# Kernel optimization log

Hardware: AMD Instinct MI355X
Metric: run time of the kernel (lower is better)

## Reference

```python
import jax, jax.numpy as jnp
import numpy as np


def setup_inputs() -> dict:
    key = jax.random.key(0)
    k1, k2 = jax.random.split(key)
    B, N, M = 4, 16384, 4096
    src_points = jax.random.normal(k1, (B, N, 3), dtype=jnp.float32)
    target_verts = jax.random.normal(k2, (B, M, 3), dtype=jnp.float32)
    return {"src_points": src_points, "target_verts": target_verts}


def reference(src_points, target_verts):
    # target_faces=None path of ChamferLoss: degenerate one-vertex triangles,
    # so closest-point-on-mesh == nearest target vertex.
    # d2[b,n,m] = ||p_bn - v_bm||^2 via the expansion p2 + v2 - 2 p.v
    p2 = jnp.sum(src_points * src_points, axis=-1)          # (B, N)
    v2 = jnp.sum(target_verts * target_verts, axis=-1)      # (B, M)
    pv = jnp.einsum('bnd,bmd->bnm', src_points, target_verts)  # (B, N, M)
    d2 = p2[:, :, None] + v2[:, None, :] - 2.0 * pv
    d2 = jnp.maximum(d2, 0.0)
    min_d2 = jnp.min(d2, axis=-1)                            # (B, N)
    num_src_per_batch = src_points.shape[1]
    loss = jnp.sum(min_d2, axis=-1) / num_src_per_batch      # (B,)
    return loss
```

## Files before the change

### kernel.cpp

```cpp
#include <hip/hip_runtime.h>
#include <float.h>


typedef __bf16 bf16x8 __attribute__((ext_vector_type(8)));
typedef float  f32x16 __attribute__((ext_vector_type(16)));

constexpr int B = 4, N = 16384, M = 4096;
constexpr int BN = B * N;
constexpr int TPB = 512;
constexpr int PPB = 256;
constexpr int NPB = BN / PPB;
constexpr int CHUNK = 2048;
constexpr int NCH = M / CHUNK;
constexpr int CT = CHUNK / 32;
constexpr int HT = CT / 2;

__global__ __launch_bounds__(TPB) void chamfer_fused(
    const float* __restrict__ src, const float* __restrict__ tv,
    float* __restrict__ out)
{
    __shared__ uint4 lds4[4096];
    char* ldsc = (char*)lds4;

    const int pblk = blockIdx.x;
    const int b    = pblk >> 6;
    const int t    = threadIdx.x;
    const int w    = t >> 6, L = t & 63;
    const int s    = w & 3, h = w >> 2;
    const int half = L >> 5, c = L & 31;
    const int laneoff = half * 512 + c * 16;

    const int P0 = pblk * PPB + s * 64;
    const int p0 = P0 + c, p1 = P0 + 32 + c;
    float x0 = src[3 * p0], y0 = src[3 * p0 + 1], z0 = src[3 * p0 + 2];
    float x1 = src[3 * p1], y1 = src[3 * p1 + 1], z1 = src[3 * p1 + 2];
    float pp0 = fmaf(x0, x0, fmaf(y0, y0, z0 * z0));
    float pp1 = fmaf(x1, x1, fmaf(y1, y1, z1 * z1));

    __bf16 one = (__bf16)1.0f, zero = (__bf16)0.0f;
    bf16x8 bP0, bP1;
    {
        __bf16 xh = (__bf16)x0, yh = (__bf16)y0, zh = (__bf16)z0;
        __bf16 xl = (__bf16)(x0 - (float)xh), yl = (__bf16)(y0 - (float)yh),
               zl = (__bf16)(z0 - (float)zh);
        if (half == 0) { bP0[0]=xh; bP0[1]=yh; bP0[2]=zh; bP0[3]=xl; bP0[4]=yl; bP0[5]=zl; bP0[6]=xh; bP0[7]=yh; }
        else { bP0[0]=zh; bP0[1]=one; bP0[2]=one; bP0[3]=zero; bP0[4]=zero; bP0[5]=zero; bP0[6]=zero; bP0[7]=zero; }
    }
    {
        __bf16 xh = (__bf16)x1, yh = (__bf16)y1, zh = (__bf16)z1;
        __bf16 xl = (__bf16)(x1 - (float)xh), yl = (__bf16)(y1 - (float)yh),
               zl = (__bf16)(z1 - (float)zh);
        if (half == 0) { bP1[0]=xh; bP1[1]=yh; bP1[2]=zh; bP1[3]=xl; bP1[4]=yl; bP1[5]=zl; bP1[6]=xh; bP1[7]=yh; }
        else { bP1[0]=zh; bP1[1]=one; bP1[2]=one; bP1[3]=zero; bP1[4]=zero; bP1[5]=zero; bP1[6]=zero; bP1[7]=zero; }
    }

    f32x16 zeroC;
#pragma unroll
    for (int r = 0; r < 16; ++r) zeroC[r] = 0.0f;
    float mn0[8], mn1[8];
#pragma unroll
    for (int u = 0; u < 8; ++u) { mn0[u] = FLT_MAX; mn1[u] = FLT_MAX; }

    for (int ch = 0; ch < NCH; ++ch) {
        if (ch) __syncthreads();

#pragma unroll
        for (int k = 0; k < 4; ++k) {
            int ml = t + k * 512;
            int i  = b * M + ch * CHUNK + ml;
            float x = tv[3 * i + 0], y = tv[3 * i + 1], z = tv[3 * i + 2];
            __bf16 xh = (__bf16)x, yh = (__bf16)y, zh = (__bf16)z;
            float xhf = (float)xh, yhf = (float)yh, zhf = (float)zh;
            __bf16 xl = (__bf16)(x - xhf), yl = (__bf16)(y - yhf),
                   zl = (__bf16)(z - zhf);
            float v2 = fmaf(x, x, fmaf(y, y, z * z));
            __bf16 v2h = (__bf16)v2;
            __bf16 v2l = (__bf16)(v2 - (float)v2h);

            bf16x8 h0, h1;
            h0[0] = (__bf16)(-2.0f * xhf); h0[1] = (__bf16)(-2.0f * yhf);
            h0[2] = (__bf16)(-2.0f * zhf);
            h0[3] = h0[0]; h0[4] = h0[1]; h0[5] = h0[2];
            h0[6] = (__bf16)(-2.0f * (float)xl); h0[7] = (__bf16)(-2.0f * (float)yl);
            h1[0] = (__bf16)(-2.0f * (float)zl); h1[1] = v2h; h1[2] = v2l;
            h1[3] = zero; h1[4] = zero; h1[5] = zero; h1[6] = zero; h1[7] = zero;

            size_t base = (size_t)(ml >> 5) * 1024 + (size_t)(ml & 31) * 16;
            *(bf16x8*)(ldsc + base)       = h0;
            *(bf16x8*)(ldsc + base + 512) = h1;
        }
        __syncthreads();

        const char* abase = ldsc + (size_t)h * (HT * 1024) + laneoff;
#pragma unroll 8
        for (int tt = 0; tt < HT; ++tt) {
            bf16x8 av = *(const bf16x8*)(abase + tt * 1024);
            f32x16 C0 = __builtin_amdgcn_mfma_f32_32x32x16_bf16(av, bP0, zeroC, 0, 0, 0);
            f32x16 C1 = __builtin_amdgcn_mfma_f32_32x32x16_bf16(av, bP1, zeroC, 0, 0, 0);
#pragma unroll
            for (int u = 0; u < 8; ++u) {
                mn0[u] = fminf(fminf(mn0[u], C0[2 * u]), C0[2 * u + 1]);
                mn1[u] = fminf(fminf(mn1[u], C1[2 * u]), C1[2 * u + 1]);
            }
        }
    }

    float a01 = fminf(fminf(mn0[0], mn0[1]), fminf(mn0[2], mn0[3]));
    float a23 = fminf(fminf(mn0[4], mn0[5]), fminf(mn0[6], mn0[7]));
    float m0 = fminf(a01, a23);
    m0 = fminf(m0, __shfl_xor(m0, 32, 64));
    float b01 = fminf(fminf(mn1[0], mn1[1]), fminf(mn1[2], mn1[3]));
    float b23 = fminf(fminf(mn1[4], mn1[5]), fminf(mn1[6], mn1[7]));
    float m1 = fminf(b01, b23);
    m1 = fminf(m1, __shfl_xor(m1, 32, 64));
    float m  = half ? m1 : m0;
    float pp = half ? pp1 : pp0;

    __syncthreads();
    float* lf = (float*)ldsc;
    float* acc = lf + 512;
    lf[t] = m;
    __syncthreads();

    float sum = 0.0f;
    if (w < 4) {
        float mm = fminf(m, lf[t + 256]);
        sum = fmaxf(mm + pp, 0.0f);
    }
    for (int off = 32; off > 0; off >>= 1)
        sum += __shfl_down(sum, off, 64);
    if (L == 0) acc[w] = sum;
    __syncthreads();
    if (t == 0) {
        float ssum = acc[0] + acc[1] + acc[2] + acc[3];
        atomicAdd(&out[b], ssum * (1.0f / N));
    }
}

extern "C" void kernel_launch(void* const* d_in, const int* in_sizes, int n_in,
                              void* d_out, int out_size, void* d_ws, size_t ws_size,
                              hipStream_t stream) {
    const float* src = (const float*)d_in[0];
    const float* tv  = (const float*)d_in[1];
    float* out = (float*)d_out;

    hipMemsetAsync(out, 0, out_size, stream);
    chamfer_fused<<<NPB, TPB, 0, stream>>>(src, tv, out);
}
```

Measured before the change: 66.83 us.

## Replace memset+atomics with cooperative grid sync reduction and prefetch next chunk

Drops the hipMemsetAsync and per-block atomicAdd. Each block now writes its partial sum to workspace, the grid synchronizes cooperatively, and the first B blocks reduce the partials into the output. It also prefetches the next chunk's target vertices into registers while the current chunk is computed. The aim is to remove a separate memset launch and to hide global load latency. The cost is a cooperative launch with a grid barrier, which requires all 256 blocks to be resident at once, plus extra registers for the prefetch.

```diff
diff --git a/kernel.cpp b/kernel.cpp
--- a/kernel.cpp
+++ b/kernel.cpp
@@ -1,5 +1,8 @@
 #include <hip/hip_runtime.h>
+#include <hip/hip_cooperative_groups.h>
 #include <float.h>
+
+namespace cg = cooperative_groups;
 
 
 typedef __bf16 bf16x8 __attribute__((ext_vector_type(8)));
@@ -15,9 +18,9 @@
 constexpr int CT = CHUNK / 32;
 constexpr int HT = CT / 2;
 
-__global__ __launch_bounds__(TPB) void chamfer_fused(
+__global__ __launch_bounds__(TPB) void chamfer_coop(
     const float* __restrict__ src, const float* __restrict__ tv,
-    float* __restrict__ out)
+    float* __restrict__ bs, float* __restrict__ out)
 {
     __shared__ uint4 lds4[4096];
     char* ldsc = (char*)lds4;
@@ -61,14 +64,21 @@
 #pragma unroll
     for (int u = 0; u < 8; ++u) { mn0[u] = FLT_MAX; mn1[u] = FLT_MAX; }
 
+    float cx[4], cy[4], cz[4], nx[4], ny[4], nz[4];
+#pragma unroll
+    for (int k = 0; k < 4; ++k) {
+        int i = b * M + t + k * 512;
+        cx[k] = tv[3 * i + 0]; cy[k] = tv[3 * i + 1]; cz[k] = tv[3 * i + 2];
+    }
+
+#pragma unroll
     for (int ch = 0; ch < NCH; ++ch) {
         if (ch) __syncthreads();
 
 #pragma unroll
         for (int k = 0; k < 4; ++k) {
             int ml = t + k * 512;
-            int i  = b * M + ch * CHUNK + ml;
-            float x = tv[3 * i + 0], y = tv[3 * i + 1], z = tv[3 * i + 2];
+            float x = cx[k], y = cy[k], z = cz[k];
             __bf16 xh = (__bf16)x, yh = (__bf16)y, zh = (__bf16)z;
             float xhf = (float)xh, yhf = (float)yh, zhf = (float)zh;
             __bf16 xl = (__bf16)(x - xhf), yl = (__bf16)(y - yhf),
@@ -89,6 +99,14 @@
             *(bf16x8*)(ldsc + base)       = h0;
             *(bf16x8*)(ldsc + base + 512) = h1;
         }
+
+        if (ch + 1 < NCH) {
+#pragma unroll
+            for (int k = 0; k < 4; ++k) {
+                int i = b * M + (ch + 1) * CHUNK + t + k * 512;
+                nx[k] = tv[3 * i + 0]; ny[k] = tv[3 * i + 1]; nz[k] = tv[3 * i + 2];
+            }
+        }
         __syncthreads();
 
         const char* abase = ldsc + (size_t)h * (HT * 1024) + laneoff;
@@ -102,6 +120,11 @@
                 mn0[u] = fminf(fminf(mn0[u], C0[2 * u]), C0[2 * u + 1]);
                 mn1[u] = fminf(fminf(mn1[u], C1[2 * u]), C1[2 * u + 1]);
             }
+        }
+
+        if (ch + 1 < NCH) {
+#pragma unroll
+            for (int k = 0; k < 4; ++k) { cx[k] = nx[k]; cy[k] = ny[k]; cz[k] = nz[k]; }
         }
     }
 
@@ -133,7 +156,16 @@
     __syncthreads();
     if (t == 0) {
         float ssum = acc[0] + acc[1] + acc[2] + acc[3];
-        atomicAdd(&out[b], ssum * (1.0f / N));
+        bs[pblk] = ssum * (1.0f / N);
+    }
+
+    cg::this_grid().sync();
+
+    if (pblk < B && w == 0) {
+        float v = bs[pblk * 64 + L];
+        for (int off = 32; off > 0; off >>= 1)
+            v += __shfl_down(v, off, 64);
+        if (L == 0) out[pblk] = v;
     }
 }
 
@@ -143,7 +175,9 @@
     const float* src = (const float*)d_in[0];
     const float* tv  = (const float*)d_in[1];
     float* out = (float*)d_out;
+    float* bs  = (float*)d_ws;
 
-    hipMemsetAsync(out, 0, out_size, stream);
-    chamfer_fused<<<NPB, TPB, 0, stream>>>(src, tv, out);
+    void* args[] = { (void*)&src, (void*)&tv, (void*)&bs, (void*)&out };
+    hipLaunchCooperativeKernel((const void*)chamfer_coop,
+                               dim3(NPB), dim3(TPB), args, 0, stream);
 }
```

Result: slower. 100.3 us (+50.2%).
